# Performance work log

Measured on AMD Instinct MI355X. Metric: run time of the kernel, lower is better.

## Reference

```python
import jax, jax.numpy as jnp
import numpy as np

HIDDEN = 1024
INTER = 4096
NUM_EXPERTS = 8
TOP_K = 2
NUM_TOKENS = 8192


def setup_inputs() -> dict:
    key = jax.random.key(0)
    k_x, k_r, k_w1, k_w2 = jax.random.split(key, 4)
    x = jax.random.normal(k_x, (NUM_TOKENS, HIDDEN), dtype=jnp.float32)
    router_w = jax.random.normal(k_r, (NUM_EXPERTS, HIDDEN), dtype=jnp.float32) * 0.02
    expert_w1 = jax.random.normal(k_w1, (NUM_EXPERTS, HIDDEN, INTER), dtype=jnp.float32) * 0.02
    # torch init: std = 0.02 / sqrt(2 * num_experts)
    expert_w2 = jax.random.normal(k_w2, (NUM_EXPERTS, INTER, HIDDEN), dtype=jnp.float32) * (0.02 / (2 * NUM_EXPERTS) ** 0.5)
    return {"x": x, "router_w": router_w, "expert_w1": expert_w1, "expert_w2": expert_w2}


def reference(x, router_w, expert_w1, expert_w2):
    num_tokens = x.shape[0]
    # Router: logits -> softmax -> top-k -> renormalize (matches torch.topk on probs)
    router_logits = x @ router_w.T                      # [T, E]
    probs = jax.nn.softmax(router_logits, axis=-1)       # [T, E]
    top_vals, top_idx = jax.lax.top_k(probs, TOP_K)      # [T, K]
    top_vals = top_vals / jnp.sum(top_vals, axis=-1, keepdims=True)

    # Auxiliary load-balancing loss (uses only the top-1 expert, as in torch code)
    expert_mask = jax.nn.one_hot(top_idx[:, 0], NUM_EXPERTS, dtype=x.dtype)  # [T, E]
    tokens_per_expert = expert_mask.sum(axis=0)                              # [E]
    router_prob = probs.mean(axis=0)                                         # [E]
    aux_loss = jnp.sum(tokens_per_expert / num_tokens * router_prob) * NUM_EXPERTS

    # Per-token combine weight for each expert (scatter top-k weights to dense [T, E])
    combine = jnp.zeros((num_tokens, NUM_EXPERTS), dtype=x.dtype)
    combine = combine.at[jnp.arange(num_tokens)[:, None], top_idx].add(top_vals)

    # Per-expert 2-layer MLP (silu), weighted combine. Loop over fixed small E.
    output = jnp.zeros_like(x)
    for e in range(NUM_EXPERTS):
        h = jax.nn.silu(x @ expert_w1[e])            # [T, I]
        output = output + combine[:, e:e + 1] * (h @ expert_w2[e])
    return output, aux_loss
```

## Files before the change

### kernel.cpp

```cpp
#include <hip/hip_runtime.h>
#include <hip/hip_bf16.h>
#include <stdint.h>

#define NTOK  8192
#define HID   1024
#define INTER 4096
#define NEXP  8
#define NSLOT (NTOK * 2)

typedef __attribute__((ext_vector_type(4))) float f32x4;
typedef __attribute__((ext_vector_type(8))) short bf16x8;
typedef __attribute__((ext_vector_type(4))) short bf16x4;

__device__ __forceinline__ short f2bf(float f) {
  union { float f; uint32_t u; } v; v.f = f;
  uint32_t u = v.u;
  u += 0x7FFFu + ((u >> 16) & 1u);
  return (short)(u >> 16);
}

__device__ __forceinline__ void glds16(const short* g, short* l) {
  __builtin_amdgcn_global_load_lds(
      (const __attribute__((address_space(1))) void*)g,
      (__attribute__((address_space(3))) void*)l, 16, 0, 0);
}

__global__ __launch_bounds__(256) void castx_k(const float* __restrict__ in,
                                               short* __restrict__ out) {
  size_t i = ((size_t)blockIdx.x * 256 + threadIdx.x) * 4;
  f32x4 v = *(const f32x4*)(in + i);
  bf16x4 o = { f2bf(v.x), f2bf(v.y), f2bf(v.z), f2bf(v.w) };
  *(bf16x4*)(out + i) = o;
}

__global__ __launch_bounds__(256) void router_k(
    const float* __restrict__ x, const float* __restrict__ rw,
    int* __restrict__ top_idx, float* __restrict__ top_w,
    float* __restrict__ probsum, float* __restrict__ cnt1) {
  __shared__ float lrw[NEXP * HID];
  __shared__ float red[4][2 * NEXP];
  int tid = threadIdx.x;
  for (int i = tid * 4; i < NEXP * HID; i += 1024)
    *(f32x4*)(lrw + i) = *(const f32x4*)(rw + i);
  __syncthreads();
  int lane = tid & 63;
  int wv = tid >> 6;
  float pacc[NEXP], cacc[NEXP];
#pragma unroll
  for (int e = 0; e < NEXP; e++) { pacc[e] = 0.f; cacc[e] = 0.f; }
#pragma unroll
  for (int it = 0; it < 4; it++) {
    int t = blockIdx.x * 16 + it * 4 + wv;
    const float* xr = x + (size_t)t * HID;
    float acc[NEXP];
#pragma unroll
    for (int e = 0; e < NEXP; e++) acc[e] = 0.f;
#pragma unroll
    for (int k4 = 0; k4 < 4; k4++) {
      int k = k4 * 256 + lane * 4;
      f32x4 xv = *(const f32x4*)(xr + k);
#pragma unroll
      for (int e = 0; e < NEXP; e++) {
        f32x4 rv = *(const f32x4*)(lrw + e * HID + k);
        acc[e] += xv.x * rv.x + xv.y * rv.y + xv.z * rv.z + xv.w * rv.w;
      }
    }
#pragma unroll
    for (int e = 0; e < NEXP; e++) {
#pragma unroll
      for (int off = 32; off > 0; off >>= 1)
        acc[e] += __shfl_xor(acc[e], off);
    }
    float mx = acc[0];
#pragma unroll
    for (int e = 1; e < NEXP; e++) mx = fmaxf(mx, acc[e]);
    float p[NEXP], s = 0.f;
#pragma unroll
    for (int e = 0; e < NEXP; e++) { p[e] = expf(acc[e] - mx); s += p[e]; }
    float inv = 1.f / s;
    float p1 = -1.f, p2 = -1.f; int i1 = 0, i2 = 0;
#pragma unroll
    for (int e = 0; e < NEXP; e++) {
      float pe = p[e] * inv;
      p[e] = pe;
      if (pe > p1)      { p2 = p1; i2 = i1; p1 = pe; i1 = e; }
      else if (pe > p2) { p2 = pe; i2 = e; }
    }
    if (lane == 0) {
      float rs = 1.f / (p1 + p2);
      top_idx[t * 2] = i1; top_idx[t * 2 + 1] = i2;
      top_w[t * 2] = p1 * rs; top_w[t * 2 + 1] = p2 * rs;
#pragma unroll
      for (int e = 0; e < NEXP; e++) {
        pacc[e] += p[e];
        cacc[e] += (i1 == e) ? 1.f : 0.f;
      }
    }
  }
  if (lane == 0) {
#pragma unroll
    for (int e = 0; e < NEXP; e++) {
      red[wv][e] = pacc[e];
      red[wv][NEXP + e] = cacc[e];
    }
  }
  __syncthreads();
  if (tid < NEXP) {
    float s = 0.f, c = 0.f;
#pragma unroll
    for (int w = 0; w < 4; w++) { s += red[w][tid]; c += red[w][NEXP + tid]; }
    atomicAdd(&probsum[tid], s);
    atomicAdd(&cnt1[tid], c);
  }
}

__global__ void aux_k(const float* probsum, const float* cnt1, float* out_aux) {
  if (threadIdx.x == 0 && blockIdx.x == 0) {
    float s = 0.f;
    for (int e = 0; e < NEXP; e++) s += cnt1[e] * probsum[e];
    out_aux[0] = s * (float)NEXP / ((float)NTOK * (float)NTOK);
  }
}

__global__ void lists_k(const int* __restrict__ top_idx, int* __restrict__ cnt,
                        int* __restrict__ lists) {
  int i = blockIdx.x * 256 + threadIdx.x;
  if (i < NSLOT) {
    int e = top_idx[i];
    int pos = atomicAdd(cnt + e, 1);
    lists[e * NTOK + pos] = i;
  }
}

__global__ __launch_bounds__(256) void transpose_k(
    const float* __restrict__ in, short* __restrict__ out, int K, int N) {
  __shared__ short tile[64][72];
  int e = blockIdx.z;
  in  += (size_t)e * K * N;
  out += (size_t)e * K * N;
  int n0 = blockIdx.x * 64, k0 = blockIdx.y * 64;
  int tid = threadIdx.x;
#pragma unroll
  for (int i = 0; i < 4; i++) {
    int k = (tid >> 4) + i * 16;
    int c = (tid & 15) * 4;
    f32x4 v = *(const f32x4*)(in + (size_t)(k0 + k) * N + n0 + c);
    tile[k][c] = f2bf(v.x); tile[k][c + 1] = f2bf(v.y);
    tile[k][c + 2] = f2bf(v.z); tile[k][c + 3] = f2bf(v.w);
  }
  __syncthreads();
#pragma unroll
  for (int i = 0; i < 2; i++) {
    int cid = tid + i * 256;
    int n = cid >> 3, kk = (cid & 7) * 8;
    bf16x8 o;
#pragma unroll
    for (int j = 0; j < 8; j++) o[j] = tile[kk + j][n];
    *(bf16x8*)(out + (size_t)(n0 + n) * K + k0 + kk) = o;
  }
}

template <int KDIM, int NDIM, bool L1>
__global__ __launch_bounds__(512, 2) void moe_gemm_k(
    const short* __restrict__ A, const short* __restrict__ Bt,
    void* __restrict__ outp, const int* __restrict__ cnt,
    const int* __restrict__ lists, const float* __restrict__ top_w) {
  constexpr int NB = NDIM / 256;
  constexpr int MB = NTOK / 256;
  constexpr int NWG = NB * MB * NEXP;
  int id = blockIdx.x;
  id = (id & 7) * (NWG >> 3) + (id >> 3);
  int n = id % NB;
  int rem = id / NB;
  int m = rem % MB;
  int e = rem / MB;

  int ce = cnt[e];
  int m0 = m * 256;
  if (m0 >= ce) return;
  int n0 = n * 256;
  const int* list = lists + e * NTOK;
  const short* B = Bt + (size_t)e * (size_t)NDIM * KDIM;

  __shared__ short As[2 * 256 * 32];
  __shared__ short Bs[2 * 256 * 32];
  __shared__ int   sSlot[256];
  __shared__ float sW[256];

  int tid = threadIdx.x;
  if (tid < 256) {
    int idx = m0 + tid;
    if (idx >= ce) idx = ce - 1;
    int slot = list[idx];
    sSlot[tid] = slot;
    sW[tid] = L1 ? 0.f : top_w[slot];
  }
  __syncthreads();

  int r1 = tid >> 2, cs = tid & 3;
  int r2 = r1 + 128;
  int q1 = (cs ^ ((r1 >> 1) & 3)) * 8;
  int q2 = (cs ^ ((r2 >> 1) & 3)) * 8;
  int ar1 = L1 ? (sSlot[r1] >> 1) : sSlot[r1];
  int ar2 = L1 ? (sSlot[r2] >> 1) : sSlot[r2];
  const short* gA1 = A + (size_t)ar1 * KDIM + q1;
  const short* gA2 = A + (size_t)ar2 * KDIM + q2;
  const short* gB1 = B + (size_t)(n0 + r1) * KDIM + q1;
  const short* gB2 = B + (size_t)(n0 + r2) * KDIM + q2;

  int lane = tid & 63, wave = tid >> 6;
  int wm = wave & 1, wn = wave >> 1;
  int lr = lane & 15, quad = lane >> 4;
  int aoff[8], boff[4];
#pragma unroll
  for (int mi = 0; mi < 8; mi++) {
    int r = wm * 128 + mi * 16 + lr;
    aoff[mi] = r * 32 + (quad ^ ((r >> 1) & 3)) * 8;
  }
#pragma unroll
  for (int ni = 0; ni < 4; ni++) {
    int nn = wn * 64 + ni * 16 + lr;
    boff[ni] = nn * 32 + (quad ^ ((nn >> 1) & 3)) * 8;
  }

  f32x4 acc[8][4] = {};

#define STAGE(BUF, KO)                                          \
  do {                                                          \
    glds16(gA1 + (KO), As + (BUF) * 8192 + tid * 8);            \
    glds16(gA2 + (KO), As + (BUF) * 8192 + 4096 + tid * 8);     \
    glds16(gB1 + (KO), Bs + (BUF) * 8192 + tid * 8);            \
    glds16(gB2 + (KO), Bs + (BUF) * 8192 + 4096 + tid * 8);     \
  } while (0)

#define KBODY(BUF, MORE, STG_T)                                               \
  do {                                                                        \
    bf16x8 af[8], bfg[4];                                                     \
    _Pragma("unroll")                                                         \
    for (int mi = 0; mi < 8; mi++)                                            \
      af[mi] = *(const bf16x8*)(As + (BUF) * 8192 + aoff[mi]);                \
    _Pragma("unroll")                                                         \
    for (int ni = 0; ni < 4; ni++)                                            \
      bfg[ni] = *(const bf16x8*)(Bs + (BUF) * 8192 + boff[ni]);               \
    asm volatile("s_waitcnt lgkmcnt(0)\n\ts_barrier" ::: "memory");           \
    if (MORE) STAGE(BUF, (STG_T) * 32);                                       \
    __builtin_amdgcn_s_setprio(1);                                            \
    _Pragma("unroll")                                                         \
    for (int mi = 0; mi < 8; mi++)                                            \
      _Pragma("unroll")                                                       \
      for (int ni = 0; ni < 4; ni++)                                          \
        acc[mi][ni] = __builtin_amdgcn_mfma_f32_16x16x32_bf16(af[mi], bfg[ni], acc[mi][ni], 0, 0, 0); \
    __builtin_amdgcn_s_setprio(0);                                            \
  } while (0)

  constexpr int NK = KDIM / 32;
  STAGE(0, 0);
  STAGE(1, 32);
  asm volatile("s_waitcnt vmcnt(4)\n\ts_barrier" ::: "memory");

#pragma unroll 1
  for (int kt = 0; kt < NK; kt += 2) {
    bool more = (kt + 2 < NK);
    KBODY(0, more, kt + 2);
    if (more) asm volatile("s_waitcnt vmcnt(4)\n\ts_barrier" ::: "memory");
    else      asm volatile("s_waitcnt vmcnt(0)\n\ts_barrier" ::: "memory");
    KBODY(1, more, kt + 3);
    if (more) asm volatile("s_waitcnt vmcnt(4)\n\ts_barrier" ::: "memory");
  }
#undef KBODY
#undef STAGE

  int ncol0 = n0 + wn * 64 + lr;
#pragma unroll
  for (int mi = 0; mi < 8; mi++) {
#pragma unroll
    for (int rg = 0; rg < 4; rg++) {
      int r = wm * 128 + mi * 16 + quad * 4 + rg;
      int gm = m0 + r;
      if (gm < ce) {
        int slot = sSlot[r];
#pragma unroll
        for (int ni = 0; ni < 4; ni++) {
          float v = acc[mi][ni][rg];
          int col = ncol0 + ni * 16;
          if (L1) {
            float sv = v / (1.f + expf(-v));
            ((short*)outp)[(size_t)slot * NDIM + col] = f2bf(sv);
          } else {
            atomicAdd((float*)outp + (size_t)(slot >> 1) * NDIM + col, v * sW[r]);
          }
        }
      }
    }
  }
}

extern "C" void kernel_launch(void* const* d_in, const int* in_sizes, int n_in,
                              void* d_out, int out_size, void* d_ws, size_t ws_size,
                              hipStream_t stream) {
  const float* x  = (const float*)d_in[0];
  const float* rw = (const float*)d_in[1];
  const float* w1 = (const float*)d_in[2];
  const float* w2 = (const float*)d_in[3];
  float* out = (float*)d_out;

  char* ws = (char*)d_ws;
  size_t off = 0;
  auto alloc = [&](size_t b) { void* p = ws + off; off += (b + 255) & ~(size_t)255; return p; };
  short* wt    = (short*)alloc((size_t)NEXP * HID * INTER * 2);
  short* h     = (short*)alloc((size_t)NSLOT * INTER * 2);
  short* xb    = (short*)alloc((size_t)NTOK * HID * 2);
  int*   tidx  = (int*)alloc(NSLOT * 4);
  float* tw    = (float*)alloc(NSLOT * 4);
  int*   lists = (int*)alloc(NEXP * NTOK * 4);
  int*   cnt   = (int*)alloc(256);
  float* probsum = (float*)(cnt + 8);
  float* cnt1    = (float*)(cnt + 16);

  hipMemsetAsync(cnt, 0, 256, stream);
  hipMemsetAsync(out, 0, (size_t)out_size * 4, stream);

  castx_k<<<(NTOK * HID / 4) / 256, 256, 0, stream>>>(x, xb);
  router_k<<<NTOK / 16, 256, 0, stream>>>(x, rw, tidx, tw, probsum, cnt1);
  aux_k<<<1, 64, 0, stream>>>(probsum, cnt1, out + (size_t)NTOK * HID);
  lists_k<<<NSLOT / 256, 256, 0, stream>>>(tidx, cnt, lists);

  transpose_k<<<dim3(INTER / 64, HID / 64, NEXP), 256, 0, stream>>>(w1, wt, HID, INTER);
  moe_gemm_k<HID, INTER, true>
      <<<(INTER / 256) * (NTOK / 256) * NEXP, 512, 0, stream>>>(
          xb, wt, h, cnt, lists, tw);

  transpose_k<<<dim3(HID / 64, INTER / 64, NEXP), 256, 0, stream>>>(w2, wt, INTER, HID);
  moe_gemm_k<INTER, HID, false>
      <<<(HID / 256) * (NTOK / 256) * NEXP, 512, 0, stream>>>(
          h, wt, out, cnt, lists, tw);
}
```

Baseline: 900.7 us.

## Deepen MoE GEMM pipeline to four LDS stages with half-tile MFMA phases

Replaces the 2-stage K=32 double buffer with four 32-wide K slices across two 64-wide buffers. Each slice is computed in two M-half phases, and the global-to-LDS loads are interleaved between phases with finer barriers, so more loads are in flight while MFMAs run. The shared slot and weight arrays and the initial __syncthreads are dropped: slot ids are now read straight from global memory in the prologue and epilogue. LDS use doubles to 64KB and the barrier count per K step rises, which may cut occupancy.

```diff
diff --git a/kernel.cpp b/kernel.cpp
--- a/kernel.cpp
+++ b/kernel.cpp
@@ -182,93 +182,100 @@
   const int* list = lists + e * NTOK;
   const short* B = Bt + (size_t)e * (size_t)NDIM * KDIM;
 
-  __shared__ short As[2 * 256 * 32];
-  __shared__ short Bs[2 * 256 * 32];
-  __shared__ int   sSlot[256];
-  __shared__ float sW[256];
+  __shared__ short As[2 * 2 * 256 * 32];
+  __shared__ short Bs[2 * 2 * 256 * 32];
 
   int tid = threadIdx.x;
-  if (tid < 256) {
-    int idx = m0 + tid;
-    if (idx >= ce) idx = ce - 1;
-    int slot = list[idx];
-    sSlot[tid] = slot;
-    sW[tid] = L1 ? 0.f : top_w[slot];
-  }
-  __syncthreads();
-
-  int r1 = tid >> 2, cs = tid & 3;
-  int r2 = r1 + 128;
-  int q1 = (cs ^ ((r1 >> 1) & 3)) * 8;
-  int q2 = (cs ^ ((r2 >> 1) & 3)) * 8;
-  int ar1 = L1 ? (sSlot[r1] >> 1) : sSlot[r1];
-  int ar2 = L1 ? (sSlot[r2] >> 1) : sSlot[r2];
-  const short* gA1 = A + (size_t)ar1 * KDIM + q1;
-  const short* gA2 = A + (size_t)ar2 * KDIM + q2;
-  const short* gB1 = B + (size_t)(n0 + r1) * KDIM + q1;
-  const short* gB2 = B + (size_t)(n0 + r2) * KDIM + q2;
+
+  int R1 = tid >> 2;
+  int R2 = R1 + 128;
+  int q  = ((tid & 3) ^ ((tid >> 3) & 3)) * 8;
+  int idx1 = m0 + R1; if (idx1 >= ce) idx1 = ce - 1;
+  int idx2 = m0 + R2; if (idx2 >= ce) idx2 = ce - 1;
+  int s1 = list[idx1], s2 = list[idx2];
+  int ar1 = L1 ? (s1 >> 1) : s1;
+  int ar2 = L1 ? (s2 >> 1) : s2;
+  const short* gA1 = A + (size_t)ar1 * KDIM + q;
+  const short* gA2 = A + (size_t)ar2 * KDIM + q;
+  const short* gB1 = B + (size_t)(n0 + R1) * KDIM + q;
+  const short* gB2 = B + (size_t)(n0 + R2) * KDIM + q;
 
   int lane = tid & 63, wave = tid >> 6;
   int wm = wave & 1, wn = wave >> 1;
   int lr = lane & 15, quad = lane >> 4;
+  int swz = (quad ^ ((lr >> 1) & 3)) * 8;
   int aoff[8], boff[4];
 #pragma unroll
-  for (int mi = 0; mi < 8; mi++) {
-    int r = wm * 128 + mi * 16 + lr;
-    aoff[mi] = r * 32 + (quad ^ ((r >> 1) & 3)) * 8;
-  }
-#pragma unroll
-  for (int ni = 0; ni < 4; ni++) {
-    int nn = wn * 64 + ni * 16 + lr;
-    boff[ni] = nn * 32 + (quad ^ ((nn >> 1) & 3)) * 8;
-  }
+  for (int mi = 0; mi < 8; mi++)
+    aoff[mi] = (wm * 128 + mi * 16 + lr) * 32 + swz;
+#pragma unroll
+  for (int ni = 0; ni < 4; ni++)
+    boff[ni] = (wn * 64 + ni * 16 + lr) * 32 + swz;
 
   f32x4 acc[8][4] = {};
 
-#define STAGE(BUF, KO)                                          \
-  do {                                                          \
-    glds16(gA1 + (KO), As + (BUF) * 8192 + tid * 8);            \
-    glds16(gA2 + (KO), As + (BUF) * 8192 + 4096 + tid * 8);     \
-    glds16(gB1 + (KO), Bs + (BUF) * 8192 + tid * 8);            \
-    glds16(gB2 + (KO), Bs + (BUF) * 8192 + 4096 + tid * 8);     \
+#define STAGE_A(BUF, KS, KO) do {                                   \
+    glds16(gA1 + (KO), As + (BUF) * 16384 + (KS) * 8192 + tid * 8); \
+    glds16(gA2 + (KO), As + (BUF) * 16384 + (KS) * 8192 + 4096 + tid * 8); \
   } while (0)
-
-#define KBODY(BUF, MORE, STG_T)                                               \
-  do {                                                                        \
-    bf16x8 af[8], bfg[4];                                                     \
+#define STAGE_B(BUF, KS, KO) do {                                   \
+    glds16(gB1 + (KO), Bs + (BUF) * 16384 + (KS) * 8192 + tid * 8); \
+    glds16(gB2 + (KO), Bs + (BUF) * 16384 + (KS) * 8192 + 4096 + tid * 8); \
+  } while (0)
+
+#define PHASE(BUF, KS, MH, ...) do {                                          \
+    const short* aP = As + (BUF) * 16384 + (KS) * 8192;                       \
+    const short* bP = Bs + (BUF) * 16384 + (KS) * 8192;                       \
+    bf16x8 af[4], bg[4];                                                      \
     _Pragma("unroll")                                                         \
-    for (int mi = 0; mi < 8; mi++)                                            \
-      af[mi] = *(const bf16x8*)(As + (BUF) * 8192 + aoff[mi]);                \
+    for (int u = 0; u < 4; u++) af[u] = *(const bf16x8*)(aP + aoff[(MH) * 4 + u]); \
     _Pragma("unroll")                                                         \
-    for (int ni = 0; ni < 4; ni++)                                            \
-      bfg[ni] = *(const bf16x8*)(Bs + (BUF) * 8192 + boff[ni]);               \
-    asm volatile("s_waitcnt lgkmcnt(0)\n\ts_barrier" ::: "memory");           \
-    if (MORE) STAGE(BUF, (STG_T) * 32);                                       \
+    for (int v = 0; v < 4; v++) bg[v] = *(const bf16x8*)(bP + boff[v]);       \
+    __VA_ARGS__;                                                              \
+    asm volatile("s_barrier" ::: "memory");                                   \
+    asm volatile("s_waitcnt lgkmcnt(0)" ::: "memory");                        \
     __builtin_amdgcn_s_setprio(1);                                            \
     _Pragma("unroll")                                                         \
-    for (int mi = 0; mi < 8; mi++)                                            \
+    for (int u = 0; u < 4; u++)                                               \
       _Pragma("unroll")                                                       \
-      for (int ni = 0; ni < 4; ni++)                                          \
-        acc[mi][ni] = __builtin_amdgcn_mfma_f32_16x16x32_bf16(af[mi], bfg[ni], acc[mi][ni], 0, 0, 0); \
+      for (int v = 0; v < 4; v++)                                             \
+        acc[(MH) * 4 + u][v] = __builtin_amdgcn_mfma_f32_16x16x32_bf16(       \
+            af[u], bg[v], acc[(MH) * 4 + u][v], 0, 0, 0);                     \
     __builtin_amdgcn_s_setprio(0);                                            \
+    asm volatile("s_barrier" ::: "memory");                                   \
   } while (0)
 
-  constexpr int NK = KDIM / 32;
-  STAGE(0, 0);
-  STAGE(1, 32);
-  asm volatile("s_waitcnt vmcnt(4)\n\ts_barrier" ::: "memory");
-
+  STAGE_A(0, 0, 0);
+  STAGE_B(0, 0, 0);
+  STAGE_A(0, 1, 32);
+  STAGE_B(0, 1, 32);
+  STAGE_A(1, 0, 64);
+  STAGE_B(1, 0, 64);
+
+  constexpr int NT = KDIM / 64;
+  constexpr int NITER = NT / 2;
 #pragma unroll 1
-  for (int kt = 0; kt < NK; kt += 2) {
-    bool more = (kt + 2 < NK);
-    KBODY(0, more, kt + 2);
-    if (more) asm volatile("s_waitcnt vmcnt(4)\n\ts_barrier" ::: "memory");
-    else      asm volatile("s_waitcnt vmcnt(0)\n\ts_barrier" ::: "memory");
-    KBODY(1, more, kt + 3);
-    if (more) asm volatile("s_waitcnt vmcnt(4)\n\ts_barrier" ::: "memory");
-  }
-#undef KBODY
-#undef STAGE
+  for (int I = 0; I < NITER; I++) {
+    int koA = I * 128;
+    bool more = (I + 1 < NITER);
+    asm volatile("s_waitcnt vmcnt(8)\ns_barrier" ::: "memory");
+    PHASE(0, 0, 0, { STAGE_A(1, 1, koA + 96); });
+    PHASE(0, 0, 1, { STAGE_B(1, 1, koA + 96); });
+    asm volatile("s_waitcnt vmcnt(8)\ns_barrier" ::: "memory");
+    PHASE(0, 1, 0, { if (more) STAGE_A(0, 0, koA + 128); });
+    PHASE(0, 1, 1, { if (more) STAGE_B(0, 0, koA + 128); });
+    if (more) asm volatile("s_waitcnt vmcnt(8)\ns_barrier" ::: "memory");
+    else      asm volatile("s_waitcnt vmcnt(4)\ns_barrier" ::: "memory");
+    PHASE(1, 0, 0, { if (more) STAGE_A(0, 1, koA + 160); });
+    PHASE(1, 0, 1, { if (more) STAGE_B(0, 1, koA + 160); });
+    if (more) asm volatile("s_waitcnt vmcnt(8)\ns_barrier" ::: "memory");
+    else      asm volatile("s_waitcnt vmcnt(0)\ns_barrier" ::: "memory");
+    PHASE(1, 1, 0, { if (more) STAGE_A(1, 0, koA + 192); });
+    PHASE(1, 1, 1, { if (more) STAGE_B(1, 0, koA + 192); });
+  }
+#undef PHASE
+#undef STAGE_A
+#undef STAGE_B
 
   int ncol0 = n0 + wn * 64 + lr;
 #pragma unroll
@@ -278,7 +285,8 @@
       int r = wm * 128 + mi * 16 + quad * 4 + rg;
       int gm = m0 + r;
       if (gm < ce) {
-        int slot = sSlot[r];
+        int slot = list[gm];
+        float w = L1 ? 0.f : top_w[slot];
 #pragma unroll
         for (int ni = 0; ni < 4; ni++) {
           float v = acc[mi][ni][rg];
@@ -287,7 +295,7 @@
             float sv = v / (1.f + expf(-v));
             ((short*)outp)[(size_t)slot * NDIM + col] = f2bf(sv);
           } else {
-            atomicAdd((float*)outp + (size_t)(slot >> 1) * NDIM + col, v * sW[r]);
+            atomicAdd((float*)outp + (size_t)(slot >> 1) * NDIM + col, v * w);
           }
         }
       }
```

After: 932.9 us. 1.04x slower.
